# Optimization experiments

Measured on AMD Instinct MI355X. Metric: run time of the kernel, lower is better.

Reference implementation:

```python
import jax, jax.numpy as jnp
import numpy as np

V, F_IN, H, DH, T = 512, 8, 64, 4, 3
E, P, L = 8192, 64, 8
D = H + DH  # path-decoder GRU width


def setup_inputs() -> dict:
    key = jax.random.key(0)
    ks = jax.random.split(key, 24)
    s = 0.1
    inp = {
        "adj_matrix": jax.random.normal(ks[0], (V, V, F_IN), jnp.float32),
        "edges": jax.random.randint(ks[1], (E, 2), 0, V),
        "paths": jax.random.randint(ks[2], (P, L), 0, V),
        "demands": jax.random.uniform(ks[3], (P,), jnp.float32),
        "emb_w": jax.random.normal(ks[4], (H, F_IN), jnp.float32) * s,
        "w1s": jax.random.normal(ks[5], (T, H, H), jnp.float32) * s,
        "w2s": jax.random.normal(ks[6], (T, H, H), jnp.float32) * s,
        "w3s": jax.random.normal(ks[7], (T, H, H), jnp.float32) * s,
        "gru_w_ih": jax.random.normal(ks[8], (3 * H, 2 * H), jnp.float32) * s,
        "gru_w_hh": jax.random.normal(ks[9], (3 * H, H), jnp.float32) * s,
        "gru_b_ih": jax.random.normal(ks[10], (3 * H,), jnp.float32) * s,
        "gru_b_hh": jax.random.normal(ks[11], (3 * H,), jnp.float32) * s,
        "pf_w_ih": jax.random.normal(ks[12], (3 * D, D), jnp.float32) * s,
        "pf_w_hh": jax.random.normal(ks[13], (3 * D, D), jnp.float32) * s,
        "pf_b_ih": jax.random.normal(ks[14], (3 * D,), jnp.float32) * s,
        "pf_b_hh": jax.random.normal(ks[15], (3 * D,), jnp.float32) * s,
        "pb_w_ih": jax.random.normal(ks[16], (3 * D, D), jnp.float32) * s,
        "pb_w_hh": jax.random.normal(ks[17], (3 * D, D), jnp.float32) * s,
        "pb_b_ih": jax.random.normal(ks[18], (3 * D,), jnp.float32) * s,
        "pb_b_hh": jax.random.normal(ks[19], (3 * D,), jnp.float32) * s,
        "wq": jax.random.normal(ks[20], (1, D), jnp.float32) * s,
        "bq": jax.random.normal(ks[21], (1,), jnp.float32) * s,
        "wd": jax.random.normal(ks[22], (DH, 1), jnp.float32) * s,
    }
    return inp


def _gru(x_seq, h0, w_ih, w_hh, b_ih, b_hh):
    """torch-style GRU, batch_first. x_seq (B,Tn,I), h0 (B,Hd) -> (ys, h_last)."""
    def step(h, x_t):
        gi = x_t @ w_ih.T + b_ih
        gh = h @ w_hh.T + b_hh
        ir, iz, inn = jnp.split(gi, 3, axis=-1)
        hr, hz, hn = jnp.split(gh, 3, axis=-1)
        r = jax.nn.sigmoid(ir + hr)
        z = jax.nn.sigmoid(iz + hz)
        n = jnp.tanh(inn + r * hn)
        h_new = (1.0 - z) * n + z * h
        return h_new, h_new
    h_last, ys = jax.lax.scan(step, h0, jnp.swapaxes(x_seq, 0, 1))
    return jnp.swapaxes(ys, 0, 1), h_last


def _message_passing(x, u, v, w1, w2, w3):
    """Vectorized form of the per-edge python loop. x (V,V,Hd), u/v (E,)."""
    Hd = x.shape[-1]
    col_sum = x.sum(axis=0)                      # (V,Hd): sum over first index
    nz_row = jnp.sum(x != 0, axis=-1)            # (V,V) nonzero count per entry
    col_nz = nz_row.sum(axis=0)                  # (V,)
    # incoming edges for edge (u,v): column u, row v zeroed, mean over nonzeros
    s_in = col_sum[u] - x[v, u]                  # (E,Hd)
    n_in = (col_nz[u] - nz_row[v, u]).astype(x.dtype) / Hd
    n_in = jnp.where(n_in == 0, 1.0, n_in)
    e_in = s_in / n_in[:, None]
    # outgoing edges: reversed edge (v,u) -> column v, row u zeroed
    s_out = col_sum[v] - x[u, v]
    n_out = (col_nz[v] - nz_row[u, v]).astype(x.dtype) / Hd
    n_out = jnp.where(n_out == 0, 1.0, n_out)
    e_out = s_out / n_out[:, None]
    m = jax.nn.relu(x[u, v] @ w1.T + e_in @ w2.T + e_out @ w3.T)
    return x.at[u, v].set(m)


def reference(adj_matrix, edges, paths, demands, emb_w, w1s, w2s, w3s,
              gru_w_ih, gru_w_hh, gru_b_ih, gru_b_hh,
              pf_w_ih, pf_w_hh, pf_b_ih, pf_b_hh,
              pb_w_ih, pb_w_hh, pb_b_ih, pb_b_hh, wq, bq, wd):
    u, v = edges[:, 0], edges[:, 1]
    x = adj_matrix @ emb_w.T                     # (V,V,H)
    for t in range(T):
        m = _message_passing(x, u, v, w1s[t], w2s[t], w3s[t])
        inp = jnp.concatenate([m, x], axis=-1)   # (V,V,2H)
        x, _ = _gru(inp, jnp.zeros((x.shape[0], H), x.dtype),
                    gru_w_ih, gru_w_hh, gru_b_ih, gru_b_hh)
    demand_emb = jax.nn.relu(demands[:, None] @ wd.T)        # (P,DH)
    graph_emb = jnp.concatenate([x.mean(axis=(0, 1)),
                                 jnp.zeros((DH,), x.dtype)])  # (D,)
    src, dst = paths[:, :-1], paths[:, 1:]                    # (P,L-1)
    edge_feat = x[src, dst]                                   # (P,L-1,H)
    dem = jnp.broadcast_to(demand_emb[:, None, :], (P, L - 1, DH))
    feat = jnp.concatenate([edge_feat, dem], axis=-1)         # (P,L-1,D)
    h0 = jnp.broadcast_to(graph_emb, (P, D))
    _, hf = _gru(feat, h0, pf_w_ih, pf_w_hh, pf_b_ih, pf_b_hh)
    _, hb = _gru(feat[:, ::-1], h0, pb_w_ih, pb_w_hh, pb_b_ih, pb_b_hh)
    paths_emb = (hf + hb) * 0.5                               # mean over directions
    return jax.nn.softmax(paths_emb @ wq.T + bq, axis=0)      # (P,1)
```

## Files before the change

kernel.cpp:

```cpp
#include <hip/hip_runtime.h>


__device__ __forceinline__ float fsig_(float x) { return 1.f / (1.f + __expf(-x)); }
__device__ __forceinline__ float ftanh_(float x) {
  float e = __expf(2.f * x);
  return 1.f - 2.f / (e + 1.f);
}
__device__ __forceinline__ float sig_(float x) { return 1.f / (1.f + expf(-x)); }

__device__ __forceinline__ void barrier_lgkm() {
  asm volatile("s_waitcnt lgkmcnt(0)\n\ts_barrier" ::: "memory");
}

#define LD4(p) (*(const float4*)(p))
#define DOT4(acc, va, vb)                                                      \
  do {                                                                         \
    acc += (va).x * (vb).x; acc += (va).y * (vb).y;                            \
    acc += (va).z * (vb).z; acc += (va).w * (vb).w;                            \
  } while (0)

#define ALL16(M) M(0) M(1) M(2) M(3) M(4) M(5) M(6) M(7)                       \
                 M(8) M(9) M(10) M(11) M(12) M(13) M(14) M(15)
#define ALLQ(M) M(0,0) M(1,1) M(2,2) M(3,3) M(4,0) M(5,1) M(6,2) M(7,3)        \
                M(8,0) M(9,1) M(10,2) M(11,3) M(12,0) M(13,1) M(14,2) M(15,3)

__global__ __launch_bounds__(256) void embed_kernel(
    const float* __restrict__ adj, const float* __restrict__ emb,
    float* __restrict__ x)
{
  const int64_t row = (int64_t)blockIdx.x * 4 + (threadIdx.x >> 6);
  const int h = threadIdx.x & 63;
  const float* a = adj + row * 8;
  float acc = 0.f;
#pragma unroll
  for (int f = 0; f < 8; ++f) acc += a[f] * emb[h * 8 + f];
  x[row * 64 + h] = acc;
}

__global__ __launch_bounds__(256) void colsum_kernel(
    const float* __restrict__ x, float* __restrict__ col_sum,
    int* __restrict__ col_nz)
{
  const int j = blockIdx.x;
  const int h = threadIdx.x & 63;
  const int w = threadIdx.x >> 6;
  float acc = 0.f;
  int nz = 0;
  for (int i = w; i < 512; i += 4) {
    float v = x[((int64_t)i * 512 + j) * 64 + h];
    acc += v;
    nz += (v != 0.f) ? 1 : 0;
  }
  __shared__ float pacc[4][64];
  __shared__ int pnz[4];
#pragma unroll
  for (int off = 32; off > 0; off >>= 1) nz += __shfl_down(nz, off, 64);
  if (h == 0) pnz[w] = nz;
  pacc[w][h] = acc;
  __syncthreads();
  if (w == 0) {
    col_sum[j * 64 + h] = pacc[0][h] + pacc[1][h] + pacc[2][h] + pacc[3][h];
    if (h == 0) col_nz[j] = pnz[0] + pnz[1] + pnz[2] + pnz[3];
  }
}

__global__ void scatter_idx_kernel(const int* __restrict__ edges,
                                   int* __restrict__ idxmap)
{
  const int e = blockIdx.x * 256 + threadIdx.x;
  if (e < 8192) idxmap[edges[e * 2] * 512 + edges[e * 2 + 1]] = e;
}

__global__ __launch_bounds__(64) void edge_kernel(
    const float* __restrict__ x, const int* __restrict__ edges,
    const float* __restrict__ col_sum, const int* __restrict__ col_nz,
    const float* __restrict__ w1, const float* __restrict__ w2,
    const float* __restrict__ w3, const float* __restrict__ w_ih,
    float* __restrict__ delta_gi)
{
  const int e = blockIdx.x;
  const int h = threadIdx.x;
  const int u = edges[e * 2 + 0];
  const int v = edges[e * 2 + 1];
  __shared__ __align__(16) float xuv[64], ein[64], eout[64], dm[64];
  const float xuvh = x[((int64_t)u * 512 + v) * 64 + h];
  const float xvuh = x[((int64_t)v * 512 + u) * 64 + h];
  xuv[h] = xuvh;
  const int nz_vu = __popcll(__ballot(xvuh != 0.f));
  const int nz_uv = __popcll(__ballot(xuvh != 0.f));
  float n_in = (float)(col_nz[u] - nz_vu) / 64.f;
  if (n_in == 0.f) n_in = 1.f;
  float n_out = (float)(col_nz[v] - nz_uv) / 64.f;
  if (n_out == 0.f) n_out = 1.f;
  ein[h] = (col_sum[u * 64 + h] - xvuh) / n_in;
  eout[h] = (col_sum[v * 64 + h] - xuvh) / n_out;
  __syncthreads();
  const float4* w1r = (const float4*)(w1 + h * 64);
  const float4* w2r = (const float4*)(w2 + h * 64);
  const float4* w3r = (const float4*)(w3 + h * 64);
  const float4* xuv4 = (const float4*)xuv;
  const float4* ein4 = (const float4*)ein;
  const float4* eout4 = (const float4*)eout;
  float acc = 0.f;
#pragma unroll
  for (int kk = 0; kk < 16; ++kk) {
    float4 a = xuv4[kk], b = w1r[kk];
    acc += a.x * b.x + a.y * b.y + a.z * b.z + a.w * b.w;
    a = ein4[kk]; b = w2r[kk];
    acc += a.x * b.x + a.y * b.y + a.z * b.z + a.w * b.w;
    a = eout4[kk]; b = w3r[kk];
    acc += a.x * b.x + a.y * b.y + a.z * b.z + a.w * b.w;
  }
  const float m = fmaxf(acc, 0.f);
  dm[h] = m - xuvh;
  __syncthreads();
  const float4* dm4 = (const float4*)dm;
#pragma unroll
  for (int r = 0; r < 3; ++r) {
    const int gg = h + r * 64;
    const float4* wr = (const float4*)(w_ih + gg * 128);
    float d = 0.f;
#pragma unroll
    for (int kk = 0; kk < 16; ++kk) {
      float4 a = dm4[kk], b = wr[kk];
      d += a.x * b.x + a.y * b.y + a.z * b.z + a.w * b.w;
    }
    delta_gi[e * 192 + gg] = d;
  }
}

#define DECL_W(i)                                                              \
  float4 W##i; {                                                               \
    float4 t0 = LD4(wg + 4 * (i));                                             \
    float4 t1 = LD4(wg + 64 + 4 * (i));                                        \
    W##i.x = t0.x + t1.x; W##i.y = t0.y + t1.y;                                \
    W##i.z = t0.z + t1.z; W##i.w = t0.w + t1.w;                                \
  }
#define DECL_X(i) float4 X##i = LD4(xrow + 4 * (i));
#define PQ(i, q) { DOT4(ac##q, X##i, W##i); X##i = LD4(xnext + 4 * (i)); }
#define DECL_WR(i) float4 WR##i = LD4(wr_ + 4 * (i));
#define DECL_WZ(i) float4 WZ##i = LD4(wz_ + 4 * (i));
#define DECL_WN(i) float4 WN##i = LD4(wn_ + 4 * (i));
#define CCHUNK(i)                                                              \
  { float4 hc = hs4[(i)];                                                      \
    DOT4(racc, hc, WR##i); DOT4(zacc, hc, WZ##i); DOT4(nacc, hc, WN##i); }

__global__ __launch_bounds__(256, 2) void scan_kernel(
    float* __restrict__ x, const float* __restrict__ delta_gi,
    const int* __restrict__ idxmap,
    const float* __restrict__ w_ih, const float* __restrict__ w_hh,
    const float* __restrict__ b_ih, const float* __restrict__ b_hh)
{
  const int b = blockIdx.x;
  const int tid = threadIdx.x;
  __shared__ __align__(16) float hs[64];
  __shared__ float gib[2][192];
  __shared__ int idxl[512];
  float* xrow = x + (int64_t)b * 32768;

  for (int i = tid; i < 512; i += 256) idxl[i] = idxmap[b * 512 + i];

  if (tid < 192) {
    const int g = tid;
    const float* wg = w_ih + g * 128;
    ALL16(DECL_W)
    const float bi = b_ih[g];
    ALL16(DECL_X)
    __syncthreads();
    {
      float ac0 = bi, ac1 = 0.f, ac2 = 0.f, ac3 = 0.f;
      const float* xnext = xrow + 64;
      ALLQ(PQ)
      float acc = (ac0 + ac1) + (ac2 + ac3);
      const int i0 = idxl[0];
      if (i0 >= 0) acc += delta_gi[(int64_t)i0 * 192 + g];
      gib[0][g] = acc;
    }
    const int idx1 = idxl[1];
    float dgn = 0.f;
    if (idx1 >= 0) dgn = delta_gi[(int64_t)idx1 * 192 + g];
    barrier_lgkm();
    for (int t = 0; t < 512; ++t) {
      if (t < 511) {
        const int tn2 = (t + 2 < 512) ? (t + 2) : 511;
        const float* xnext = xrow + tn2 * 64;
        float ac0 = bi + dgn, ac1 = 0.f, ac2 = 0.f, ac3 = 0.f;
        ALLQ(PQ)
        gib[(t + 1) & 1][g] = (ac0 + ac1) + (ac2 + ac3);
        const int idxn = idxl[tn2];
        dgn = 0.f;
        if (idxn >= 0) dgn = delta_gi[(int64_t)idxn * 192 + g];
      }
      barrier_lgkm();
    }
  } else {
    const int j = tid - 192;
    const float* wr_ = w_hh + j * 64;
    const float* wz_ = w_hh + (j + 64) * 64;
    const float* wn_ = w_hh + (j + 128) * 64;
    ALL16(DECL_WR)
    ALL16(DECL_WZ)
    ALL16(DECL_WN)
    const float bhr = b_hh[j], bhz = b_hh[j + 64], bhn = b_hh[j + 128];
    float hj = 0.f;
    hs[j] = 0.f;
    __syncthreads();
    barrier_lgkm();
    const float4* hs4 = (const float4*)hs;
    for (int t = 0; t < 512; ++t) {
      const float gr = gib[t & 1][j];
      const float gz = gib[t & 1][64 + j];
      const float gn = gib[t & 1][128 + j];
      float racc = bhr, zacc = bhz, nacc = bhn;
      ALL16(CCHUNK)
      const float r = fsig_(gr + racc);
      const float z = fsig_(gz + zacc);
      const float n = ftanh_(gn + r * nacc);
      hj = (1.f - z) * n + z * hj;
      hs[j] = hj;
      xrow[t * 64 + j] = hj;
      barrier_lgkm();
    }
  }
}

__global__ __launch_bounds__(64) void graphemb_kernel(
    const float* __restrict__ col_sum, float* __restrict__ graph_emb)
{
  const int h = threadIdx.x;
  float s = 0.f;
#pragma unroll 8
  for (int j = 0; j < 512; ++j) s += col_sum[j * 64 + h];
  graph_emb[h] = s * (1.f / 262144.f);
  if (h < 4) graph_emb[64 + h] = 0.f;
}

__global__ __launch_bounds__(256) void path_kernel(
    const float* __restrict__ x, const int* __restrict__ paths,
    const float* __restrict__ demands, const float* __restrict__ wd,
    const float* __restrict__ graph_emb,
    const float* __restrict__ wih_f, const float* __restrict__ whh_f,
    const float* __restrict__ bih_f, const float* __restrict__ bhh_f,
    const float* __restrict__ wih_b, const float* __restrict__ whh_b,
    const float* __restrict__ bih_b, const float* __restrict__ bhh_b,
    float* __restrict__ h_out)
{
  const int p = blockIdx.x & 63;
  const int dir = blockIdx.x >> 6;
  const int g = threadIdx.x;
  const float* w_ih = dir ? wih_b : wih_f;
  const float* w_hh = dir ? whh_b : whh_f;
  const float* bih = dir ? bih_b : bih_f;
  const float* bhh = dir ? bhh_b : bhh_f;
  __shared__ float feat[7][68], hs[68], rbuf[68], zbuf[68];
  if (g < 68) {
#pragma unroll
    for (int t = 0; t < 7; ++t) {
      const int src = paths[p * 8 + t];
      const int dst = paths[p * 8 + t + 1];
      feat[t][g] = (g < 64) ? x[((int64_t)src * 512 + dst) * 64 + g]
                            : fmaxf(demands[p] * wd[g - 64], 0.f);
    }
    hs[g] = graph_emb[g];
  }
  __syncthreads();
  for (int s = 0; s < 7; ++s) {
    const int t = dir ? (6 - s) : s;
    float acc = 0.f, hacc = 0.f;
    if (g < 204) {
      acc = bih[g];
      hacc = bhh[g];
      for (int k = 0; k < 68; ++k) {
        acc += feat[t][k] * w_ih[g * 68 + k];
        hacc += hs[k] * w_hh[g * 68 + k];
      }
    }
    if (g < 68) rbuf[g] = sig_(acc + hacc);
    else if (g < 136) zbuf[g - 68] = sig_(acc + hacc);
    __syncthreads();
    if (g >= 136 && g < 204) {
      const int j = g - 136;
      const float n = tanhf(acc + rbuf[j] * hacc);
      const float z = zbuf[j];
      const float hn = (1.f - z) * n + z * hs[j];
      hs[j] = hn;
    }
    __syncthreads();
  }
  if (g < 68) h_out[(dir * 64 + p) * 68 + g] = hs[g];
}

__global__ __launch_bounds__(64) void combine_kernel(
    const float* __restrict__ h_out, const float* __restrict__ wq,
    const float* __restrict__ bq, float* __restrict__ out)
{
  const int p = threadIdx.x;
  float l = bq[0];
#pragma unroll
  for (int d = 0; d < 68; ++d)
    l += 0.5f * (h_out[p * 68 + d] + h_out[(64 + p) * 68 + d]) * wq[d];
  float mx = l;
#pragma unroll
  for (int off = 32; off > 0; off >>= 1) mx = fmaxf(mx, __shfl_xor(mx, off, 64));
  const float e = expf(l - mx);
  float s = e;
#pragma unroll
  for (int off = 32; off > 0; off >>= 1) s += __shfl_xor(s, off, 64);
  out[p] = e / s;
}

extern "C" void kernel_launch(void* const* d_in, const int* in_sizes, int n_in,
                              void* d_out, int out_size, void* d_ws, size_t ws_size,
                              hipStream_t stream)
{
  const float* adj = (const float*)d_in[0];
  const int* edges = (const int*)d_in[1];
  const int* paths = (const int*)d_in[2];
  const float* demands = (const float*)d_in[3];
  const float* emb_w = (const float*)d_in[4];
  const float* w1s = (const float*)d_in[5];
  const float* w2s = (const float*)d_in[6];
  const float* w3s = (const float*)d_in[7];
  const float* gru_w_ih = (const float*)d_in[8];
  const float* gru_w_hh = (const float*)d_in[9];
  const float* gru_b_ih = (const float*)d_in[10];
  const float* gru_b_hh = (const float*)d_in[11];
  const float* pf_w_ih = (const float*)d_in[12];
  const float* pf_w_hh = (const float*)d_in[13];
  const float* pf_b_ih = (const float*)d_in[14];
  const float* pf_b_hh = (const float*)d_in[15];
  const float* pb_w_ih = (const float*)d_in[16];
  const float* pb_w_hh = (const float*)d_in[17];
  const float* pb_b_ih = (const float*)d_in[18];
  const float* pb_b_hh = (const float*)d_in[19];
  const float* wq = (const float*)d_in[20];
  const float* bq = (const float*)d_in[21];
  const float* wd = (const float*)d_in[22];
  float* out = (float*)d_out;

  float* xA = (float*)d_ws;
  float* col_sum = xA + 16777216;
  int* col_nz = (int*)(col_sum + 32768);
  int* idxmap = col_nz + 512;
  float* delta_gi = (float*)(idxmap + 262144);
  float* graph_emb = delta_gi + 1572864;
  float* h_out = graph_emb + 128;

  hipMemsetAsync(idxmap, 0xFF, 262144 * sizeof(int), stream);
  scatter_idx_kernel<<<32, 256, 0, stream>>>(edges, idxmap);
  embed_kernel<<<65536, 256, 0, stream>>>(adj, emb_w, xA);

  for (int t = 0; t < 3; ++t) {
    colsum_kernel<<<512, 256, 0, stream>>>(xA, col_sum, col_nz);
    edge_kernel<<<8192, 64, 0, stream>>>(xA, edges, col_sum, col_nz,
        w1s + t * 4096, w2s + t * 4096, w3s + t * 4096, gru_w_ih, delta_gi);
    scan_kernel<<<512, 256, 0, stream>>>(xA, delta_gi, idxmap,
        gru_w_ih, gru_w_hh, gru_b_ih, gru_b_hh);
  }

  colsum_kernel<<<512, 256, 0, stream>>>(xA, col_sum, col_nz);
  graphemb_kernel<<<1, 64, 0, stream>>>(col_sum, graph_emb);
  path_kernel<<<128, 256, 0, stream>>>(xA, paths, demands, wd, graph_emb,
      pf_w_ih, pf_w_hh, pf_b_ih, pf_b_hh,
      pb_w_ih, pb_w_hh, pb_b_ih, pb_b_hh, h_out);
  combine_kernel<<<1, 64, 0, stream>>>(h_out, wq, bq, out);
}
```

Baseline: 1.987 ms.

## Split GRU hidden gates across waves and batch input projections from an LDS ring

```diff
diff --git a/kernel.cpp b/kernel.cpp
--- a/kernel.cpp
+++ b/kernel.cpp
@@ -11,6 +11,13 @@
 __device__ __forceinline__ void barrier_lgkm() {
   asm volatile("s_waitcnt lgkmcnt(0)\n\ts_barrier" ::: "memory");
 }
+
+#define PIN4(v) asm volatile("" : "+v"((v).x), "+v"((v).y), "+v"((v).z), "+v"((v).w))
+
+#define GLD_LDS4(gp, lp)                                                       \
+  __builtin_amdgcn_global_load_lds(                                            \
+      (const __attribute__((address_space(1))) void*)(gp),                     \
+      (__attribute__((address_space(3))) void*)(lp), 4, 0, 0)
 
 #define LD4(p) (*(const float4*)(p))
 #define DOT4(acc, va, vb)                                                      \
@@ -129,21 +136,57 @@
   }
 }
 
-#define DECL_W(i)                                                              \
-  float4 W##i; {                                                               \
-    float4 t0 = LD4(wg + 4 * (i));                                             \
-    float4 t1 = LD4(wg + 64 + 4 * (i));                                        \
-    W##i.x = t0.x + t1.x; W##i.y = t0.y + t1.y;                                \
-    W##i.z = t0.z + t1.z; W##i.w = t0.w + t1.w;                                \
-  }
-#define DECL_X(i) float4 X##i = LD4(xrow + 4 * (i));
-#define PQ(i, q) { DOT4(ac##q, X##i, W##i); X##i = LD4(xnext + 4 * (i)); }
-#define DECL_WR(i) float4 WR##i = LD4(wr_ + 4 * (i));
-#define DECL_WZ(i) float4 WZ##i = LD4(wz_ + 4 * (i));
-#define DECL_WN(i) float4 WN##i = LD4(wn_ + 4 * (i));
-#define CCHUNK(i)                                                              \
-  { float4 hc = hs4[(i)];                                                      \
-    DOT4(racc, hc, WR##i); DOT4(zacc, hc, WZ##i); DOT4(nacc, hc, WN##i); }
+#define DECL_WC(i) float4 WC##i = LD4(wc + 4 * (i)); PIN4(WC##i);
+#define HQ(i, q) { float4 hc = hs4[(i)]; DOT4(hh##q, hc, WC##i); }
+
+#define GIBATCH(ga, gb, gc, gd, tbase)                                         \
+  {                                                                            \
+    const int sA = ((tbase) + 1) & 15, sB = ((tbase) + 2) & 15;                \
+    const int sC = ((tbase) + 3) & 15, sD = ((tbase) + 4) & 15;                \
+    ga = bi; gb = bi; gc = bi; gd = bi;                                        \
+    _Pragma("unroll")                                                          \
+    for (int q = 0; q < 16; ++q) {                                             \
+      const float4 va = *(const float4*)&xring[sA][4 * q];                     \
+      const float4 vb = *(const float4*)&xring[sB][4 * q];                     \
+      const float4 vc = *(const float4*)&xring[sC][4 * q];                     \
+      const float4 vd = *(const float4*)&xring[sD][4 * q];                     \
+      const float w0 = wsumT[4 * q + 0][g];                                    \
+      const float w1 = wsumT[4 * q + 1][g];                                    \
+      const float w2 = wsumT[4 * q + 2][g];                                    \
+      const float w3 = wsumT[4 * q + 3][g];                                    \
+      ga += va.x * w0 + va.y * w1 + va.z * w2 + va.w * w3;                     \
+      gb += vb.x * w0 + vb.y * w1 + vb.z * w2 + vb.w * w3;                     \
+      gc += vc.x * w0 + vc.y * w1 + vc.z * w2 + vc.w * w3;                     \
+      gd += vd.x * w0 + vd.y * w1 + vd.z * w2 + vd.w * w3;                     \
+    }                                                                          \
+    { const int i1 = idxl[(tbase) + 1];                                        \
+      if (i1 >= 0) ga += delta_gi[(int64_t)i1 * 192 + g];                      \
+      const int i2 = idxl[(tbase) + 2];                                        \
+      if (i2 >= 0) gb += delta_gi[(int64_t)i2 * 192 + g];                      \
+      const int i3 = idxl[(tbase) + 3];                                        \
+      if (i3 >= 0) gc += delta_gi[(int64_t)i3 * 192 + g];                      \
+      const int i4 = ((tbase) + 4 < 512) ? idxl[(tbase) + 4] : -1;             \
+      if (i4 >= 0) gd += delta_gi[(int64_t)i4 * 192 + g]; }                    \
+  }
+
+#define HSTEP(gcur, tcur)                                                      \
+  {                                                                            \
+    float hh0 = bc, hh1 = 0.f, hh2 = 0.f, hh3 = 0.f;                           \
+    ALLQ(HQ)                                                                   \
+    const float gh = (hh0 + hh1) + (hh2 + hh3);                                \
+    if (tau == 0) rzb[0][j] = fsig_((gcur) + gh);                              \
+    else if (tau == 1) rzb[1][j] = fsig_((gcur) + gh);                         \
+    barrier_lgkm();                                     \
+    if (tau == 2) {                                                            \
+      const float r = rzb[0][j];                                               \
+      const float z = rzb[1][j];                                               \
+      const float n = ftanh_((gcur) + r * gh);                                 \
+      hj = (1.f - z) * n + z * hj;                                             \
+      hsb[j] = hj;                                                             \
+      xrow[(tcur) * 64 + j] = hj;                                              \
+    }                                                                          \
+    barrier_lgkm();                                       \
+  }
 
 __global__ __launch_bounds__(256, 2) void scan_kernel(
     float* __restrict__ x, const float* __restrict__ delta_gi,
@@ -151,74 +194,72 @@
     const float* __restrict__ w_ih, const float* __restrict__ w_hh,
     const float* __restrict__ b_ih, const float* __restrict__ b_hh)
 {
+  const int tid = threadIdx.x;
   const int b = blockIdx.x;
-  const int tid = threadIdx.x;
-  __shared__ __align__(16) float hs[64];
-  __shared__ float gib[2][192];
+  __shared__ __align__(16) float wsumT[64][192];
+  __shared__ __align__(16) float xring[16][64];
+  __shared__ float hsb[64];
+  __shared__ float rzb[2][64];
   __shared__ int idxl[512];
   float* xrow = x + (int64_t)b * 32768;
 
+  for (int i = tid; i < 12288; i += 256) {
+    const int k = i >> 7;
+    const int kk = i / 192, gg = i - kk * 192;
+    (void)k;
+    wsumT[kk][gg] = w_ih[gg * 128 + kk] + w_ih[gg * 128 + 64 + kk];
+  }
   for (int i = tid; i < 512; i += 256) idxl[i] = idxmap[b * 512 + i];
+  if (tid < 64) hsb[tid] = 0.f;
+  if (tid >= 192) {
+    const int lane = tid & 63;
+#pragma unroll
+    for (int s = 0; s < 8; ++s)
+      GLD_LDS4(xrow + s * 64 + lane, &xring[s][0]);
+  }
+  __syncthreads();
 
   if (tid < 192) {
     const int g = tid;
-    const float* wg = w_ih + g * 128;
-    ALL16(DECL_W)
+    const int j = tid & 63;
+    const int tau = tid >> 6;
+    const float* wc = w_hh + g * 64;
+    ALL16(DECL_WC)
     const float bi = b_ih[g];
-    ALL16(DECL_X)
-    __syncthreads();
+    const float bc = b_hh[g];
+    const float4* hs4 = (const float4*)hsb;
+    float hj = 0.f;
+    float g0;
     {
-      float ac0 = bi, ac1 = 0.f, ac2 = 0.f, ac3 = 0.f;
-      const float* xnext = xrow + 64;
-      ALLQ(PQ)
-      float acc = (ac0 + ac1) + (ac2 + ac3);
+      float s0 = bi, s1 = 0.f, s2 = 0.f, s3 = 0.f;
+#pragma unroll
+      for (int q = 0; q < 16; ++q) {
+        const float4 va = *(const float4*)&xring[0][4 * q];
+        s0 += va.x * wsumT[4 * q + 0][g];
+        s1 += va.y * wsumT[4 * q + 1][g];
+        s2 += va.z * wsumT[4 * q + 2][g];
+        s3 += va.w * wsumT[4 * q + 3][g];
+      }
+      g0 = (s0 + s1) + (s2 + s3);
       const int i0 = idxl[0];
-      if (i0 >= 0) acc += delta_gi[(int64_t)i0 * 192 + g];
-      gib[0][g] = acc;
-    }
-    const int idx1 = idxl[1];
-    float dgn = 0.f;
-    if (idx1 >= 0) dgn = delta_gi[(int64_t)idx1 * 192 + g];
-    barrier_lgkm();
+      if (i0 >= 0) g0 += delta_gi[(int64_t)i0 * 192 + g];
+    }
+    float g1, g2, g3, g4;
+    for (int t = 0; t < 512; t += 4) {
+      GIBATCH(g1, g2, g3, g4, t)
+      HSTEP(g0, t)
+      HSTEP(g1, t + 1)
+      HSTEP(g2, t + 2)
+      HSTEP(g3, t + 3)
+      g0 = g4;
+    }
+  } else {
+    const int lane = tid & 63;
     for (int t = 0; t < 512; ++t) {
-      if (t < 511) {
-        const int tn2 = (t + 2 < 512) ? (t + 2) : 511;
-        const float* xnext = xrow + tn2 * 64;
-        float ac0 = bi + dgn, ac1 = 0.f, ac2 = 0.f, ac3 = 0.f;
-        ALLQ(PQ)
-        gib[(t + 1) & 1][g] = (ac0 + ac1) + (ac2 + ac3);
-        const int idxn = idxl[tn2];
-        dgn = 0.f;
-        if (idxn >= 0) dgn = delta_gi[(int64_t)idxn * 192 + g];
-      }
+      const int tf = (t + 8 < 512) ? (t + 8) : 511;
+      GLD_LDS4(xrow + tf * 64 + lane, &xring[(t + 8) & 15][0]);
+      asm volatile("s_waitcnt vmcnt(3)" ::: "memory");
       barrier_lgkm();
-    }
-  } else {
-    const int j = tid - 192;
-    const float* wr_ = w_hh + j * 64;
-    const float* wz_ = w_hh + (j + 64) * 64;
-    const float* wn_ = w_hh + (j + 128) * 64;
-    ALL16(DECL_WR)
-    ALL16(DECL_WZ)
-    ALL16(DECL_WN)
-    const float bhr = b_hh[j], bhz = b_hh[j + 64], bhn = b_hh[j + 128];
-    float hj = 0.f;
-    hs[j] = 0.f;
-    __syncthreads();
-    barrier_lgkm();
-    const float4* hs4 = (const float4*)hs;
-    for (int t = 0; t < 512; ++t) {
-      const float gr = gib[t & 1][j];
-      const float gz = gib[t & 1][64 + j];
-      const float gn = gib[t & 1][128 + j];
-      float racc = bhr, zacc = bhz, nacc = bhn;
-      ALL16(CCHUNK)
-      const float r = fsig_(gr + racc);
-      const float z = fsig_(gz + zacc);
-      const float n = ftanh_(gn + r * nacc);
-      hj = (1.f - z) * n + z * hj;
-      hs[j] = hj;
-      xrow[t * 64 + j] = hj;
       barrier_lgkm();
     }
   }
```

Result: slower. 4.234 ms (+113.0%).
